# Performance work log

Hardware: AMD Instinct MI355X
Metric: run time of the kernel (lower is better)

## Reference

```python
import jax, jax.numpy as jnp
import numpy as np

N, D, NUM_CLASSES = 8192, 256, 512
DELTA = 1.0


def setup_inputs() -> dict:
    key = jax.random.key(0)
    k1, k2 = jax.random.split(key)
    queries = jax.random.normal(k1, (N, D), dtype=jnp.float32)
    targets = jax.random.randint(k2, (N,), 0, NUM_CLASSES, dtype=jnp.int64)
    return {"queries": queries, "targets": targets}


def _mine(queries, targets):
    # Pairwise squared L2 distances via gram expansion (avoids [N,N,D] intermediate).
    sq = jnp.sum(queries * queries, axis=-1)              # [N]
    dist = sq[:, None] + sq[None, :] - 2.0 * (queries @ queries.T)  # [N,N]
    same = targets[:, None] == targets[None, :]           # [N,N] bool
    diag = jnp.eye(dist.shape[0], dtype=bool)
    neg_inf = jnp.float32(-jnp.inf)
    # hardest positive: argmax over (distances * same_mask) with -inf diagonal
    pos_masked = jnp.where(diag, neg_inf, dist * same)
    pos_idx = jnp.argmax(pos_masked, axis=-1)
    # original: (-(distances * ~same, diag=-inf)).argmin == argmax of the masked matrix
    neg_masked = jnp.where(diag, neg_inf, dist * (~same))
    neg_idx = jnp.argmax(neg_masked, axis=-1)
    return pos_idx, neg_idx


def reference(queries, targets):
    pos_idx, neg_idx = _mine(queries, targets)
    pos = queries[pos_idx]                                # [N,D]
    neg = queries[neg_idx]                                # [N,D]
    d_pos = jnp.sum((queries - pos) ** 2, axis=-1, keepdims=True)  # [N,1]
    d_neg = jnp.sum((queries - neg) ** 2, axis=-1, keepdims=True)  # [N,1]
    loss = jax.nn.relu(DELTA - d_pos + d_neg)
    return jnp.mean(loss)
```

## Files before the change

### kernel.cpp

```cpp
#include <hip/hip_runtime.h>

#define N 8192
#define D 256
#define NB 64
#define NTILES (NB * (NB + 1) / 2)

typedef float f32x4 __attribute__((ext_vector_type(4)));
typedef long long i64;

__device__ __forceinline__ void gload16(const void* g, void* lds) {
    __builtin_amdgcn_global_load_lds(
        (const __attribute__((address_space(1))) void*)g,
        (__attribute__((address_space(3))) void*)lds, 16, 0, 0);
}


__global__ __launch_bounds__(256) void prep_kernel(const float* __restrict__ q,
                                                   unsigned char* __restrict__ q8,
                                                   float* __restrict__ sq,
                                                   unsigned* __restrict__ pos_key,
                                                   unsigned* __restrict__ neg_key,
                                                   float* __restrict__ out) {
    const int row = blockIdx.x * 4 + (threadIdx.x >> 6);
    const int lane = threadIdx.x & 63;
    if (threadIdx.x < 8) {
        const int r0 = blockIdx.x * 4 + (threadIdx.x >> 1);
        if (threadIdx.x & 1) neg_key[r0] = 0u; else pos_key[r0] = 0u;
    }
    if (blockIdx.x == 0 && threadIdx.x == 0) out[0] = 0.0f;
    const float4 v = ((const float4*)(q + row * D))[lane];
    int r = 0;
    r = __builtin_amdgcn_cvt_pk_fp8_f32(v.x, v.y, r, false);
    r = __builtin_amdgcn_cvt_pk_fp8_f32(v.z, v.w, r, true);
    ((int*)(q8 + (size_t)row * D))[lane] = r;
    float s = v.x * v.x + v.y * v.y + v.z * v.z + v.w * v.w;
    #pragma unroll
    for (int off = 32; off; off >>= 1) s += __shfl_down(s, off, 64);
    if (lane == 0) sq[row] = s;
}

__global__ __launch_bounds__(256, 3) void mine_kernel(
    const unsigned char* __restrict__ q8, const int* __restrict__ tgt,
    const float* __restrict__ sqv,
    unsigned* __restrict__ pos_key, unsigned* __restrict__ neg_key)
{
    __shared__ __align__(16) unsigned Msh[2 * 128 * 33];
    __shared__ float sqI[128], sqJ[128];
    __shared__ int   tgI[128], tgJ[128];
    char* const smem = (char*)Msh;

    int tt = blockIdx.x, bi = 0;
    while (tt >= NB - bi) { tt -= NB - bi; ++bi; }
    const int bj = bi + tt;
    const int i0 = bi * 128, j0 = bj * 128;
    const bool diag = (bi == bj);

    const int tid = threadIdx.x;
    const int w = tid >> 6, lane = tid & 63;
    const int quad = lane >> 4, lc = lane & 15;
    const int wy = w >> 1, wx = w & 1;

    if (tid < 128) { sqI[tid] = sqv[i0 + tid]; tgI[tid] = tgt[i0 + tid]; }
    else { const int c = tid - 128; sqJ[c] = sqv[j0 + c]; tgJ[c] = tgt[j0 + c]; }
    __syncthreads();

    float sqjn[4];
    #pragma unroll
    for (int nt = 0; nt < 4; ++nt) sqjn[nt] = sqJ[wx * 64 + nt * 16 + lc];
    f32x4 acc[4][4];
    #pragma unroll
    for (int mt = 0; mt < 4; ++mt) {
        const f32x4 si4 = *(const f32x4*)&sqI[wy * 64 + mt * 16 + quad * 4];
        #pragma unroll
        for (int nt = 0; nt < 4; ++nt)
            #pragma unroll
            for (int r = 0; r < 4; ++r)
                acc[mt][nt][r] = -0.5f * (si4[r] + sqjn[nt]);
    }

    for (int c = 0; c < D / 64; ++c) {
        const int dkb = c * 64;
        __syncthreads();
        #pragma unroll
        for (int it = 0; it < 2; ++it) {
            const int s = it * 256 + tid;
            const int r = s >> 2, bo = (s & 3) * 16;
            const int lbase = (it * 256 + w * 64) * 16;
            gload16(q8 + (size_t)(i0 + r) * D + dkb + bo, smem + lbase);
            if (!diag)
                gload16(q8 + (size_t)(j0 + r) * D + dkb + bo, smem + 8192 + lbase);
        }
        __syncthreads();

        const char* AP = smem;
        const char* BP = diag ? AP : smem + 8192;
        union { int4 v; i64 d[2]; } fb[4], fa;
        #pragma unroll
        for (int t = 0; t < 4; ++t)
            fb[t].v = *(const int4*)(BP + (wx * 64 + t * 16 + lc) * 64 + quad * 16);
        #pragma unroll
        for (int mt = 0; mt < 4; ++mt) {
            fa.v = *(const int4*)(AP + (wy * 64 + mt * 16 + lc) * 64 + quad * 16);
            #pragma unroll
            for (int nt = 0; nt < 4; ++nt) {
                acc[mt][nt] = __builtin_amdgcn_mfma_f32_16x16x32_fp8_fp8(
                    fa.d[0], fb[nt].d[0], acc[mt][nt], 0, 0, 0);
                acc[mt][nt] = __builtin_amdgcn_mfma_f32_16x16x32_fp8_fp8(
                    fa.d[1], fb[nt].d[1], acc[mt][nt], 0, 0, 0);
            }
        }
    }
    __syncthreads();

    unsigned* const mpos = Msh;
    unsigned* const mneg = Msh + 128 * 33;

    int tj[4]; unsigned jc[4], jpk[4], jnk[4];
    #pragma unroll
    for (int nt = 0; nt < 4; ++nt) {
        const int cl = wx * 64 + nt * 16 + lc;
        tj[nt] = tgJ[cl];
        jc[nt] = 0x1FFFu - (unsigned)(j0 + cl);
        jpk[nt] = 0u; jnk[nt] = 0u;
    }

    #pragma unroll
    for (int mt = 0; mt < 4; ++mt) {
        const int rbase = wy * 64 + mt * 16 + quad * 4;
        const int4 ti4 = *(const int4*)&tgI[rbase];
        #pragma unroll
        for (int r = 0; r < 4; ++r) {
            const int sr = rbase + r;
            const unsigned rk = 0x1FFFu - (unsigned)(i0 + sr);
            const int ti = ((const int*)&ti4)[r];
            unsigned bpk = 0u, bnk = 0u;
            #pragma unroll
            for (int nt = 0; nt < 4; ++nt) {
                const int cl = wx * 64 + nt * 16 + lc;
                const float dist = fmaxf(-2.0f * acc[mt][nt][r], 0.0f);
                const unsigned db = __float_as_uint(dist) & 0xFFFFE000u;
                const bool same = (ti == tj[nt]);
                const bool dia = diag && (sr == cl);
                const unsigned pb_ = dia ? 0u : (same ? db : 0u);
                const unsigned nb_ = dia ? 0u : (same ? 0u : db);
                bpk = max(bpk, dia ? 0u : (pb_ | jc[nt]));
                bnk = max(bnk, dia ? 0u : (nb_ | jc[nt]));
                jpk[nt] = max(jpk[nt], dia ? 0u : (pb_ | rk));
                jnk[nt] = max(jnk[nt], dia ? 0u : (nb_ | rk));
            }
            mpos[sr * 33 + wx * 16 + lc] = bpk;
            mneg[sr * 33 + wx * 16 + lc] = bnk;
        }
    }
    __syncthreads();

    {
        const int sr = tid & 127;
        const unsigned* m = (tid < 128) ? &mpos[sr * 33] : &mneg[sr * 33];
        unsigned best = 0u;
        #pragma unroll
        for (int k = 0; k < 32; ++k) best = max(best, m[k]);
        unsigned* gk = (tid < 128) ? pos_key : neg_key;
        atomicMax(&gk[i0 + sr], best);
    }

    if (!diag) {
        #pragma unroll
        for (int nt = 0; nt < 4; ++nt) {
            unsigned pk = jpk[nt], nk = jnk[nt];
            #pragma unroll
            for (int off = 16; off < 64; off <<= 1) {
                pk = max(pk, (unsigned)__shfl_xor((int)pk, off, 64));
                nk = max(nk, (unsigned)__shfl_xor((int)nk, off, 64));
            }
            if (quad == 0) {
                const int gcol = j0 + wx * 64 + nt * 16 + lc;
                atomicMax(&pos_key[gcol], pk);
                atomicMax(&neg_key[gcol], nk);
            }
        }
    }
}

__global__ __launch_bounds__(256) void final_kernel(
    const float* __restrict__ q, const unsigned* __restrict__ pos_key,
    const unsigned* __restrict__ neg_key, float* __restrict__ out)
{
    __shared__ float red[4];
    const int wv = threadIdx.x >> 6, lane = threadIdx.x & 63;
    float wsum = 0.0f;
    for (int rr = 0; rr < 32; ++rr) {
        const int row = (blockIdx.x * 4 + wv) * 32 + rr;
        const int bpi = 0x1FFF - (int)(pos_key[row] & 0x1FFFu);
        const int bni = 0x1FFF - (int)(neg_key[row] & 0x1FFFu);
        const float4 qi = ((const float4*)(q + row * D))[lane];
        const float4 qp = ((const float4*)(q + (size_t)bpi * D))[lane];
        const float4 qn = ((const float4*)(q + (size_t)bni * D))[lane];
        float dx, dp = 0.0f, dn = 0.0f;
        dx = qi.x - qp.x; dp += dx * dx;
        dx = qi.y - qp.y; dp += dx * dx;
        dx = qi.z - qp.z; dp += dx * dx;
        dx = qi.w - qp.w; dp += dx * dx;
        dx = qi.x - qn.x; dn += dx * dx;
        dx = qi.y - qn.y; dn += dx * dx;
        dx = qi.z - qn.z; dn += dx * dx;
        dx = qi.w - qn.w; dn += dx * dx;
        #pragma unroll
        for (int off = 32; off; off >>= 1) {
            dp += __shfl_down(dp, off, 64);
            dn += __shfl_down(dn, off, 64);
        }
        if (lane == 0) wsum += fmaxf(0.0f, (1.0f - dp) + dn);
    }
    if (lane == 0) red[wv] = wsum;
    __syncthreads();
    if (threadIdx.x == 0)
        atomicAdd(out, (red[0] + red[1] + red[2] + red[3]) * (1.0f / N));
}

extern "C" void kernel_launch(void* const* d_in, const int* in_sizes, int n_in,
                              void* d_out, int out_size, void* d_ws, size_t ws_size,
                              hipStream_t stream) {
    const float* q = (const float*)d_in[0];
    const int* tgt = (const int*)d_in[1];
    float* out = (float*)d_out;

    unsigned* pos_key = (unsigned*)d_ws;
    unsigned* neg_key = pos_key + N;
    unsigned char* q8 = (unsigned char*)(neg_key + N);
    float* sqv = (float*)(q8 + (size_t)N * D);

    prep_kernel<<<dim3(N / 4), dim3(256), 0, stream>>>(q, q8, sqv, pos_key, neg_key, out);
    mine_kernel<<<dim3(NTILES), dim3(256), 0, stream>>>(q8, tgt, sqv, pos_key, neg_key);
    final_kernel<<<dim3(64), dim3(256), 0, stream>>>(q, pos_key, neg_key, out);
}
```

Before: 106.7 us.

## Double-buffer fp8 tile loads in mining kernel and widen final kernel grid

The mining kernel now uses two LDS buffers, prefetching the next 64-wide K chunk with async global-to-LDS loads while MFMAs run on the current chunk. It uses raw waitcnt/barrier sequences and raises wave priority around the MFMA block. Diagonal tiles now also load the B half instead of reusing A, which adds redundant traffic. The final kernel handles 4 rows per wave over 512 blocks instead of 32 rows over 64 blocks, giving more parallelism at the cost of more atomics.

```diff
diff --git a/kernel.cpp b/kernel.cpp
--- a/kernel.cpp
+++ b/kernel.cpp
@@ -60,9 +60,23 @@
     const int quad = lane >> 4, lc = lane & 15;
     const int wy = w >> 1, wx = w & 1;
 
+#define STAGE(cc, bb) do {                                                   \
+        const int _dk = (cc) * 64;                                           \
+        { const int _s = tid; const int _r = _s >> 2, _bo = (_s & 3) * 16;   \
+          const int _lb = (bb) * 16384 + (w * 64) * 16;                      \
+          gload16(q8 + (size_t)(i0 + _r) * D + _dk + _bo, smem + _lb);       \
+          gload16(q8 + (size_t)(j0 + _r) * D + _dk + _bo, smem + 8192 + _lb); } \
+        { const int _s = 256 + tid; const int _r = _s >> 2, _bo = (_s & 3) * 16; \
+          const int _lb = (bb) * 16384 + (256 + w * 64) * 16;                \
+          gload16(q8 + (size_t)(i0 + _r) * D + _dk + _bo, smem + _lb);       \
+          gload16(q8 + (size_t)(j0 + _r) * D + _dk + _bo, smem + 8192 + _lb); } \
+    } while (0)
+
     if (tid < 128) { sqI[tid] = sqv[i0 + tid]; tgI[tid] = tgt[i0 + tid]; }
     else { const int c = tid - 128; sqJ[c] = sqv[j0 + c]; tgJ[c] = tgt[j0 + c]; }
-    __syncthreads();
+
+    STAGE(0, 0);
+    asm volatile("s_waitcnt lgkmcnt(0)\n\ts_barrier" ::: "memory");
 
     float sqjn[4];
     #pragma unroll
@@ -78,26 +92,21 @@
                 acc[mt][nt][r] = -0.5f * (si4[r] + sqjn[nt]);
     }
 
-    for (int c = 0; c < D / 64; ++c) {
-        const int dkb = c * 64;
-        __syncthreads();
-        #pragma unroll
-        for (int it = 0; it < 2; ++it) {
-            const int s = it * 256 + tid;
-            const int r = s >> 2, bo = (s & 3) * 16;
-            const int lbase = (it * 256 + w * 64) * 16;
-            gload16(q8 + (size_t)(i0 + r) * D + dkb + bo, smem + lbase);
-            if (!diag)
-                gload16(q8 + (size_t)(j0 + r) * D + dkb + bo, smem + 8192 + lbase);
-        }
-        __syncthreads();
-
-        const char* AP = smem;
-        const char* BP = diag ? AP : smem + 8192;
+    #pragma unroll
+    for (int c = 0; c < 4; ++c) {
+        if (c < 3) {
+            STAGE(c + 1, (c + 1) & 1);
+            asm volatile("s_waitcnt vmcnt(4)\n\ts_barrier" ::: "memory");
+        } else {
+            asm volatile("s_waitcnt vmcnt(0)\n\ts_barrier" ::: "memory");
+        }
+        const char* AP = smem + (c & 1) * 16384;
+        const char* BP = AP + 8192;
         union { int4 v; i64 d[2]; } fb[4], fa;
         #pragma unroll
         for (int t = 0; t < 4; ++t)
             fb[t].v = *(const int4*)(BP + (wx * 64 + t * 16 + lc) * 64 + quad * 16);
+        __builtin_amdgcn_s_setprio(1);
         #pragma unroll
         for (int mt = 0; mt < 4; ++mt) {
             fa.v = *(const int4*)(AP + (wy * 64 + mt * 16 + lc) * 64 + quad * 16);
@@ -109,8 +118,10 @@
                     fa.d[1], fb[nt].d[1], acc[mt][nt], 0, 0, 0);
             }
         }
-    }
-    __syncthreads();
+        __builtin_amdgcn_s_setprio(0);
+        asm volatile("s_waitcnt lgkmcnt(0)\n\ts_barrier" ::: "memory");
+    }
+#undef STAGE
 
     unsigned* const mpos = Msh;
     unsigned* const mneg = Msh + 128 * 33;
@@ -189,8 +200,9 @@
     __shared__ float red[4];
     const int wv = threadIdx.x >> 6, lane = threadIdx.x & 63;
     float wsum = 0.0f;
-    for (int rr = 0; rr < 32; ++rr) {
-        const int row = (blockIdx.x * 4 + wv) * 32 + rr;
+    #pragma unroll
+    for (int rr = 0; rr < 4; ++rr) {
+        const int row = (blockIdx.x * 4 + wv) * 4 + rr;
         const int bpi = 0x1FFF - (int)(pos_key[row] & 0x1FFFu);
         const int bni = 0x1FFF - (int)(neg_key[row] & 0x1FFFu);
         const float4 qi = ((const float4*)(q + row * D))[lane];
@@ -232,5 +244,5 @@
 
     prep_kernel<<<dim3(N / 4), dim3(256), 0, stream>>>(q, q8, sqv, pos_key, neg_key, out);
     mine_kernel<<<dim3(NTILES), dim3(256), 0, stream>>>(q8, tgt, sqv, pos_key, neg_key);
-    final_kernel<<<dim3(64), dim3(256), 0, stream>>>(q, pos_key, neg_key, out);
-}
+    final_kernel<<<dim3(512), dim3(256), 0, stream>>>(q, pos_key, neg_key, out);
+}
```

Result: faster. 100.1 us (-6.2%).
